# Performance work log

Measured on AMD Instinct MI355X. Metric: run time of the kernel, lower is better.

Reference implementation:

```python
import jax, jax.numpy as jnp
import numpy as np

B, H, S, D = 4, 16, 2048, 128

def setup_inputs() -> dict:
    key = jax.random.key(0)
    kq, kk, kv = jax.random.split(key, 3)
    query = jax.random.normal(kq, (B, H, S, D), dtype=jnp.float32)
    k = jax.random.normal(kk, (B, H, S, D), dtype=jnp.float32)
    value = jax.random.normal(kv, (B, H, S, D), dtype=jnp.float32)
    attn_mask = jnp.zeros((B, H, S, S), dtype=jnp.float32)
    return {"query": query, "key": k, "value": value, "attn_mask": attn_mask}

def reference(query, key, value, attn_mask):
    # scores: [B,H,S,S]
    scale = 1.0 / jnp.sqrt(jnp.asarray(query.shape[-1], query.dtype))
    scores = jnp.einsum('bhqd,bhkd->bhqk', query, key) * scale + attn_mask
    attn = jax.nn.softmax(scores, axis=-1)
    out = jnp.einsum('bhqk,bhkd->bhqd', attn, value)
    return out
```

## Files before the change

### kernel.cpp

```cpp
#include <hip/hip_runtime.h>

#define SDIM 2048
#define DDIM 128
#define NBH  64
#define BR   128
#define BC   64
#define PSTRIDE 72

using bf16x8 = __attribute__((ext_vector_type(8))) short;
using f32x4  = __attribute__((ext_vector_type(4))) float;

static __device__ __forceinline__ short f2bf(float x) {
    unsigned u = __float_as_uint(x);
    u += 0x7fff + ((u >> 16) & 1);
    return (short)(u >> 16);
}
static __device__ __forceinline__ unsigned pack2(float a, float b) {
    return ((unsigned)(unsigned short)f2bf(a)) |
           (((unsigned)(unsigned short)f2bf(b)) << 16);
}

__global__ __launch_bounds__(256) void kconv_kernel(const float* __restrict__ K,
                                                    unsigned short* __restrict__ Kc)
{
    size_t i = ((size_t)blockIdx.x * 256 + threadIdx.x) * 4;
    float4 v = *(const float4*)(K + i);
    uint2 o;
    o.x = pack2(v.x, v.y);
    o.y = pack2(v.z, v.w);
    *(uint2*)(Kc + i) = o;
}

__global__ __launch_bounds__(256) void vtrans_kernel(const float* __restrict__ V,
                                                     unsigned short* __restrict__ Vt)
{
    __shared__ float t[32][33];
    const int bh = blockIdx.z;
    const int s0 = blockIdx.x * 32;
    const int d0 = blockIdx.y * 32;
    const int x = threadIdx.x & 31;
    const int y = threadIdx.x >> 5;
    const float* Vb = V + (size_t)bh * SDIM * DDIM;
    unsigned short* Vtb = Vt + (size_t)bh * SDIM * DDIM;
#pragma unroll
    for (int i = 0; i < 4; ++i) {
        int r = y + i * 8;
        t[r][x] = Vb[(size_t)(s0 + r) * DDIM + d0 + x];
    }
    __syncthreads();
#pragma unroll
    for (int i = 0; i < 4; ++i) {
        int r = y + i * 8;
        Vtb[(size_t)(d0 + r) * SDIM + s0 + x] = (unsigned short)f2bf(t[x][r]);
    }
}

__global__ __launch_bounds__(256, 2) void fattn_kernel(
    const float* __restrict__ Q, const float* __restrict__ M,
    const unsigned short* __restrict__ Kc, const unsigned short* __restrict__ Vt,
    float* __restrict__ O)
{
    const int qt   = blockIdx.x;
    const int bh   = blockIdx.y;
    const int tid  = threadIdx.x;
    const int wave = tid >> 6;
    const int lane = tid & 63;
    const int quad = lane >> 4;
    const int n16  = lane & 15;
    const int q0   = qt * BR;

    const float* Qb = Q + (size_t)bh * SDIM * DDIM;
    const float* Mb = M + (size_t)bh * SDIM * SDIM;
    const unsigned short* Kb = Kc + (size_t)bh * SDIM * DDIM;
    const unsigned short* Vb = Vt + (size_t)bh * SDIM * DDIM;
    float* Ob = O + (size_t)bh * SDIM * DDIM;

    __shared__ __align__(16) unsigned short Ps[4][32 * PSTRIDE];

    const float scale = 0.08838834764831845f;
    bf16x8 qf[2][4];
#pragma unroll
    for (int rt = 0; rt < 2; ++rt) {
        int row = q0 + wave * 32 + rt * 16 + n16;
        const float* qp = Qb + (size_t)row * DDIM + quad * 8;
#pragma unroll
        for (int dt = 0; dt < 4; ++dt) {
            const float* p = qp + dt * 32;
            float4 a = *(const float4*)p;
            float4 b = *(const float4*)(p + 4);
            bf16x8 f;
            f[0] = f2bf(a.x * scale); f[1] = f2bf(a.y * scale);
            f[2] = f2bf(a.z * scale); f[3] = f2bf(a.w * scale);
            f[4] = f2bf(b.x * scale); f[5] = f2bf(b.y * scale);
            f[6] = f2bf(b.z * scale); f[7] = f2bf(b.w * scale);
            qf[rt][dt] = f;
        }
    }

    f32x4 acc[2][8];
    const f32x4 zero4 = {0.f, 0.f, 0.f, 0.f};
#pragma unroll
    for (int rt = 0; rt < 2; ++rt)
#pragma unroll
        for (int nt = 0; nt < 8; ++nt) acc[rt][nt] = zero4;
    float mrow[2][4], lrow[2][4];
#pragma unroll
    for (int rt = 0; rt < 2; ++rt)
#pragma unroll
        for (int r = 0; r < 4; ++r) { mrow[rt][r] = -1e30f; lrow[rt][r] = 0.f; }

    for (int k0 = 0; k0 < SDIM; k0 += BC) {
        float mk[2][4][4];
#pragma unroll
        for (int rt = 0; rt < 2; ++rt) {
            int rowb = q0 + wave * 32 + rt * 16 + quad * 4;
            const float* mpb = Mb + (size_t)rowb * SDIM + k0 + n16;
#pragma unroll
            for (int ct = 0; ct < 4; ++ct)
#pragma unroll
                for (int r = 0; r < 4; ++r)
                    mk[rt][ct][r] = mpb[(size_t)r * SDIM + ct * 16];
        }

        f32x4 s[2][4];
#pragma unroll
        for (int rt = 0; rt < 2; ++rt)
#pragma unroll
            for (int ct = 0; ct < 4; ++ct) s[rt][ct] = zero4;
#pragma unroll
        for (int dt = 0; dt < 4; ++dt) {
#pragma unroll
            for (int ct = 0; ct < 4; ++ct) {
                bf16x8 kf = *(const bf16x8*)(Kb + (size_t)(k0 + ct * 16 + n16) * DDIM + dt * 32 + quad * 8);
                s[0][ct] = __builtin_amdgcn_mfma_f32_16x16x32_bf16(qf[0][dt], kf, s[0][ct], 0, 0, 0);
                s[1][ct] = __builtin_amdgcn_mfma_f32_16x16x32_bf16(qf[1][dt], kf, s[1][ct], 0, 0, 0);
            }
        }

#pragma unroll
        for (int rt = 0; rt < 2; ++rt)
#pragma unroll
            for (int ct = 0; ct < 4; ++ct)
#pragma unroll
                for (int r = 0; r < 4; ++r)
                    s[rt][ct][r] += mk[rt][ct][r];

        float mx[2][4];
#pragma unroll
        for (int rt = 0; rt < 2; ++rt)
#pragma unroll
            for (int r = 0; r < 4; ++r)
                mx[rt][r] = fmaxf(fmaxf(s[rt][0][r], s[rt][1][r]),
                                  fmaxf(s[rt][2][r], s[rt][3][r]));
#pragma unroll
        for (int st = 1; st <= 8; st <<= 1)
#pragma unroll
            for (int rt = 0; rt < 2; ++rt)
#pragma unroll
                for (int r = 0; r < 4; ++r)
                    mx[rt][r] = fmaxf(mx[rt][r], __shfl_xor(mx[rt][r], st));

        float al[2][4], rs[2][4];
#pragma unroll
        for (int rt = 0; rt < 2; ++rt)
#pragma unroll
            for (int r = 0; r < 4; ++r) {
                float mnew = fmaxf(mrow[rt][r], mx[rt][r]);
                al[rt][r] = exp2f((mrow[rt][r] - mnew) * 1.44269504f);
                mrow[rt][r] = mnew;
                float t = 0.f;
#pragma unroll
                for (int ct = 0; ct < 4; ++ct) {
                    float pv = exp2f((s[rt][ct][r] - mnew) * 1.44269504f);
                    s[rt][ct][r] = pv;
                    t += pv;
                }
                rs[rt][r] = t;
            }
#pragma unroll
        for (int st = 1; st <= 8; st <<= 1)
#pragma unroll
            for (int rt = 0; rt < 2; ++rt)
#pragma unroll
                for (int r = 0; r < 4; ++r)
                    rs[rt][r] += __shfl_xor(rs[rt][r], st);
#pragma unroll
        for (int rt = 0; rt < 2; ++rt)
#pragma unroll
            for (int r = 0; r < 4; ++r) {
                lrow[rt][r] = lrow[rt][r] * al[rt][r] + rs[rt][r];
#pragma unroll
                for (int nt = 0; nt < 8; ++nt) acc[rt][nt][r] *= al[rt][r];
            }

#pragma unroll
        for (int rt = 0; rt < 2; ++rt)
#pragma unroll
            for (int ct = 0; ct < 4; ++ct)
#pragma unroll
                for (int r = 0; r < 4; ++r)
                    Ps[wave][(rt * 16 + (lane >> 4) * 4 + r) * PSTRIDE + ct * 16 + n16] =
                        (unsigned short)f2bf(s[rt][ct][r]);

        bf16x8 pa[2][2];
#pragma unroll
        for (int rt = 0; rt < 2; ++rt)
#pragma unroll
            for (int kt = 0; kt < 2; ++kt)
                pa[rt][kt] = *(const bf16x8*)(&Ps[wave][(rt * 16 + n16) * PSTRIDE + kt * 32 + quad * 8]);

#pragma unroll
        for (int nt = 0; nt < 8; ++nt) {
#pragma unroll
            for (int kt = 0; kt < 2; ++kt) {
                bf16x8 vf = *(const bf16x8*)(Vb + (size_t)(nt * 16 + n16) * SDIM + k0 + kt * 32 + quad * 8);
                acc[0][nt] = __builtin_amdgcn_mfma_f32_16x16x32_bf16(pa[0][kt], vf, acc[0][nt], 0, 0, 0);
                acc[1][nt] = __builtin_amdgcn_mfma_f32_16x16x32_bf16(pa[1][kt], vf, acc[1][nt], 0, 0, 0);
            }
        }
    }

#pragma unroll
    for (int rt = 0; rt < 2; ++rt) {
#pragma unroll
        for (int r = 0; r < 4; ++r) {
            float inv = 1.0f / lrow[rt][r];
            int row = q0 + wave * 32 + rt * 16 + quad * 4 + r;
            float* op = Ob + (size_t)row * DDIM + n16;
#pragma unroll
            for (int nt = 0; nt < 8; ++nt)
                op[nt * 16] = acc[rt][nt][r] * inv;
        }
    }
}

extern "C" void kernel_launch(void* const* d_in, const int* in_sizes, int n_in,
                              void* d_out, int out_size, void* d_ws, size_t ws_size,
                              hipStream_t stream) {
    const float* Q = (const float*)d_in[0];
    const float* K = (const float*)d_in[1];
    const float* V = (const float*)d_in[2];
    const float* M = (const float*)d_in[3];
    float* O = (float*)d_out;

    unsigned short* Kc = (unsigned short*)d_ws;
    unsigned short* Vt = Kc + (size_t)NBH * SDIM * DDIM;

    size_t nElem = (size_t)NBH * SDIM * DDIM;
    kconv_kernel<<<dim3(nElem / (256 * 4)), 256, 0, stream>>>(K, Kc);
    vtrans_kernel<<<dim3(SDIM / 32, DDIM / 32, NBH), 256, 0, stream>>>(V, Vt);

    dim3 grid(SDIM / BR, NBH);
    fattn_kernel<<<grid, 256, 0, stream>>>(Q, M, Kc, Vt, O);
}
```

Measured before the change: 1.974 ms.

## Prefetch mask tiles one step ahead, skip unchanged-max rescale, remap grid for locality

Measured after the change: 1.983 ms. About the same (+0.5%).

```diff
diff --git a/kernel.cpp b/kernel.cpp
--- a/kernel.cpp
+++ b/kernel.cpp
@@ -55,13 +55,159 @@
     }
 }
 
+static __device__ __forceinline__ void load_mask(const float* __restrict__ Mb,
+                                                 int q0, int wave, int quad, int n16,
+                                                 int kcol, float (&mk)[2][4][4])
+{
+#pragma unroll
+    for (int rt = 0; rt < 2; ++rt) {
+        const int rowb = q0 + wave * 32 + rt * 16 + quad * 4;
+        const float* mpb = Mb + (size_t)rowb * SDIM + kcol + n16;
+#pragma unroll
+        for (int ct = 0; ct < 4; ++ct)
+#pragma unroll
+            for (int r = 0; r < 4; ++r)
+                mk[rt][ct][r] = mpb[(size_t)r * SDIM + ct * 16];
+    }
+}
+
+static __device__ __forceinline__ void ktile_body(
+    int k0, int q0, int wave, int quad, int n16, int lane,
+    const float* __restrict__ Mb,
+    const unsigned short* __restrict__ Kb, const unsigned short* __restrict__ Vb,
+    unsigned short* __restrict__ PsW,
+    const bf16x8 (&qf)[2][4],
+    f32x4 (&acc)[2][8], float (&mrow)[2][4], float (&lrow)[2][4],
+    float (&mkc)[2][4][4], float (&mkn)[2][4][4])
+{
+    const f32x4 zero4 = {0.f, 0.f, 0.f, 0.f};
+
+    f32x4 s[2][4];
+#pragma unroll
+    for (int rt = 0; rt < 2; ++rt)
+#pragma unroll
+        for (int ct = 0; ct < 4; ++ct) s[rt][ct] = zero4;
+#pragma unroll
+    for (int dt = 0; dt < 4; ++dt) {
+#pragma unroll
+        for (int ct = 0; ct < 4; ++ct) {
+            bf16x8 kf = *(const bf16x8*)(Kb + (size_t)(k0 + ct * 16 + n16) * DDIM + dt * 32 + quad * 8);
+            s[0][ct] = __builtin_amdgcn_mfma_f32_16x16x32_bf16(qf[0][dt], kf, s[0][ct], 0, 0, 0);
+            s[1][ct] = __builtin_amdgcn_mfma_f32_16x16x32_bf16(qf[1][dt], kf, s[1][ct], 0, 0, 0);
+        }
+    }
+
+    __builtin_amdgcn_sched_barrier(0);
+    load_mask(Mb, q0, wave, quad, n16, (k0 + BC) & (SDIM - 1), mkn);
+    __builtin_amdgcn_sched_barrier(0);
+
+#pragma unroll
+    for (int rt = 0; rt < 2; ++rt)
+#pragma unroll
+        for (int ct = 0; ct < 4; ++ct)
+#pragma unroll
+            for (int r = 0; r < 4; ++r)
+                s[rt][ct][r] += mkc[rt][ct][r];
+
+    float mx[2][4];
+#pragma unroll
+    for (int rt = 0; rt < 2; ++rt)
+#pragma unroll
+        for (int r = 0; r < 4; ++r)
+            mx[rt][r] = fmaxf(fmaxf(s[rt][0][r], s[rt][1][r]),
+                              fmaxf(s[rt][2][r], s[rt][3][r]));
+#pragma unroll
+    for (int st = 1; st <= 8; st <<= 1)
+#pragma unroll
+        for (int rt = 0; rt < 2; ++rt)
+#pragma unroll
+            for (int r = 0; r < 4; ++r)
+                mx[rt][r] = fmaxf(mx[rt][r], __shfl_xor(mx[rt][r], st));
+
+    int anynew = 0;
+#pragma unroll
+    for (int rt = 0; rt < 2; ++rt)
+#pragma unroll
+        for (int r = 0; r < 4; ++r)
+            anynew |= (mx[rt][r] > mrow[rt][r]) ? 1 : 0;
+    if (__ballot(anynew) != 0ull) {
+#pragma unroll
+        for (int rt = 0; rt < 2; ++rt)
+#pragma unroll
+            for (int r = 0; r < 4; ++r) {
+                float mnew = fmaxf(mrow[rt][r], mx[rt][r]);
+                float al = exp2f((mrow[rt][r] - mnew) * 1.44269504f);
+                mrow[rt][r] = mnew;
+                lrow[rt][r] *= al;
+#pragma unroll
+                for (int nt = 0; nt < 8; ++nt) acc[rt][nt][r] *= al;
+            }
+    }
+
+    float rs[2][4];
+#pragma unroll
+    for (int rt = 0; rt < 2; ++rt)
+#pragma unroll
+        for (int r = 0; r < 4; ++r) {
+            float t = 0.f;
+#pragma unroll
+            for (int ct = 0; ct < 4; ++ct) {
+                float pv = exp2f((s[rt][ct][r] - mrow[rt][r]) * 1.44269504f);
+                s[rt][ct][r] = pv;
+                t += pv;
+            }
+            rs[rt][r] = t;
+        }
+#pragma unroll
+    for (int st = 1; st <= 8; st <<= 1)
+#pragma unroll
+        for (int rt = 0; rt < 2; ++rt)
+#pragma unroll
+            for (int r = 0; r < 4; ++r)
+                rs[rt][r] += __shfl_xor(rs[rt][r], st);
+#pragma unroll
+    for (int rt = 0; rt < 2; ++rt)
+#pragma unroll
+        for (int r = 0; r < 4; ++r)
+            lrow[rt][r] += rs[rt][r];
+
+#pragma unroll
+    for (int rt = 0; rt < 2; ++rt)
+#pragma unroll
+        for (int ct = 0; ct < 4; ++ct)
+#pragma unroll
+            for (int r = 0; r < 4; ++r)
+                PsW[(rt * 16 + (lane >> 4) * 4 + r) * PSTRIDE + ct * 16 + n16] =
+                    (unsigned short)f2bf(s[rt][ct][r]);
+
+    bf16x8 pa[2][2];
+#pragma unroll
+    for (int rt = 0; rt < 2; ++rt)
+#pragma unroll
+        for (int kt = 0; kt < 2; ++kt)
+            pa[rt][kt] = *(const bf16x8*)(&PsW[(rt * 16 + n16) * PSTRIDE + kt * 32 + quad * 8]);
+
+#pragma unroll
+    for (int nt = 0; nt < 8; ++nt) {
+#pragma unroll
+        for (int kt = 0; kt < 2; ++kt) {
+            bf16x8 vf = *(const bf16x8*)(Vb + (size_t)(nt * 16 + n16) * SDIM + k0 + kt * 32 + quad * 8);
+            acc[0][nt] = __builtin_amdgcn_mfma_f32_16x16x32_bf16(pa[0][kt], vf, acc[0][nt], 0, 0, 0);
+            acc[1][nt] = __builtin_amdgcn_mfma_f32_16x16x32_bf16(pa[1][kt], vf, acc[1][nt], 0, 0, 0);
+        }
+    }
+}
+
 __global__ __launch_bounds__(256, 2) void fattn_kernel(
     const float* __restrict__ Q, const float* __restrict__ M,
     const unsigned short* __restrict__ Kc, const unsigned short* __restrict__ Vt,
     float* __restrict__ O)
 {
-    const int qt   = blockIdx.x;
-    const int bh   = blockIdx.y;
+    const int flat = blockIdx.x;
+    const int slot = flat >> 3;
+    const int bh   = (flat & 7) * 8 + (slot >> 4);
+    const int qt   = slot & 15;
+
     const int tid  = threadIdx.x;
     const int wave = tid >> 6;
     const int lane = tid & 63;
@@ -76,6 +222,7 @@
     float* Ob = O + (size_t)bh * SDIM * DDIM;
 
     __shared__ __align__(16) unsigned short Ps[4][32 * PSTRIDE];
+    unsigned short* PsW = Ps[wave];
 
     const float scale = 0.08838834764831845f;
     bf16x8 qf[2][4];
@@ -109,115 +256,15 @@
 #pragma unroll
         for (int r = 0; r < 4; ++r) { mrow[rt][r] = -1e30f; lrow[rt][r] = 0.f; }
 
-    for (int k0 = 0; k0 < SDIM; k0 += BC) {
-        float mk[2][4][4];
-#pragma unroll
-        for (int rt = 0; rt < 2; ++rt) {
-            int rowb = q0 + wave * 32 + rt * 16 + quad * 4;
-            const float* mpb = Mb + (size_t)rowb * SDIM + k0 + n16;
-#pragma unroll
-            for (int ct = 0; ct < 4; ++ct)
-#pragma unroll
-                for (int r = 0; r < 4; ++r)
-                    mk[rt][ct][r] = mpb[(size_t)r * SDIM + ct * 16];
-        }
-
-        f32x4 s[2][4];
-#pragma unroll
-        for (int rt = 0; rt < 2; ++rt)
-#pragma unroll
-            for (int ct = 0; ct < 4; ++ct) s[rt][ct] = zero4;
-#pragma unroll
-        for (int dt = 0; dt < 4; ++dt) {
-#pragma unroll
-            for (int ct = 0; ct < 4; ++ct) {
-                bf16x8 kf = *(const bf16x8*)(Kb + (size_t)(k0 + ct * 16 + n16) * DDIM + dt * 32 + quad * 8);
-                s[0][ct] = __builtin_amdgcn_mfma_f32_16x16x32_bf16(qf[0][dt], kf, s[0][ct], 0, 0, 0);
-                s[1][ct] = __builtin_amdgcn_mfma_f32_16x16x32_bf16(qf[1][dt], kf, s[1][ct], 0, 0, 0);
-            }
-        }
-
-#pragma unroll
-        for (int rt = 0; rt < 2; ++rt)
-#pragma unroll
-            for (int ct = 0; ct < 4; ++ct)
-#pragma unroll
-                for (int r = 0; r < 4; ++r)
-                    s[rt][ct][r] += mk[rt][ct][r];
-
-        float mx[2][4];
-#pragma unroll
-        for (int rt = 0; rt < 2; ++rt)
-#pragma unroll
-            for (int r = 0; r < 4; ++r)
-                mx[rt][r] = fmaxf(fmaxf(s[rt][0][r], s[rt][1][r]),
-                                  fmaxf(s[rt][2][r], s[rt][3][r]));
-#pragma unroll
-        for (int st = 1; st <= 8; st <<= 1)
-#pragma unroll
-            for (int rt = 0; rt < 2; ++rt)
-#pragma unroll
-                for (int r = 0; r < 4; ++r)
-                    mx[rt][r] = fmaxf(mx[rt][r], __shfl_xor(mx[rt][r], st));
-
-        float al[2][4], rs[2][4];
-#pragma unroll
-        for (int rt = 0; rt < 2; ++rt)
-#pragma unroll
-            for (int r = 0; r < 4; ++r) {
-                float mnew = fmaxf(mrow[rt][r], mx[rt][r]);
-                al[rt][r] = exp2f((mrow[rt][r] - mnew) * 1.44269504f);
-                mrow[rt][r] = mnew;
-                float t = 0.f;
-#pragma unroll
-                for (int ct = 0; ct < 4; ++ct) {
-                    float pv = exp2f((s[rt][ct][r] - mnew) * 1.44269504f);
-                    s[rt][ct][r] = pv;
-                    t += pv;
-                }
-                rs[rt][r] = t;
-            }
-#pragma unroll
-        for (int st = 1; st <= 8; st <<= 1)
-#pragma unroll
-            for (int rt = 0; rt < 2; ++rt)
-#pragma unroll
-                for (int r = 0; r < 4; ++r)
-                    rs[rt][r] += __shfl_xor(rs[rt][r], st);
-#pragma unroll
-        for (int rt = 0; rt < 2; ++rt)
-#pragma unroll
-            for (int r = 0; r < 4; ++r) {
-                lrow[rt][r] = lrow[rt][r] * al[rt][r] + rs[rt][r];
-#pragma unroll
-                for (int nt = 0; nt < 8; ++nt) acc[rt][nt][r] *= al[rt][r];
-            }
-
-#pragma unroll
-        for (int rt = 0; rt < 2; ++rt)
-#pragma unroll
-            for (int ct = 0; ct < 4; ++ct)
-#pragma unroll
-                for (int r = 0; r < 4; ++r)
-                    Ps[wave][(rt * 16 + (lane >> 4) * 4 + r) * PSTRIDE + ct * 16 + n16] =
-                        (unsigned short)f2bf(s[rt][ct][r]);
-
-        bf16x8 pa[2][2];
-#pragma unroll
-        for (int rt = 0; rt < 2; ++rt)
-#pragma unroll
-            for (int kt = 0; kt < 2; ++kt)
-                pa[rt][kt] = *(const bf16x8*)(&Ps[wave][(rt * 16 + n16) * PSTRIDE + kt * 32 + quad * 8]);
-
-#pragma unroll
-        for (int nt = 0; nt < 8; ++nt) {
-#pragma unroll
-            for (int kt = 0; kt < 2; ++kt) {
-                bf16x8 vf = *(const bf16x8*)(Vb + (size_t)(nt * 16 + n16) * SDIM + k0 + kt * 32 + quad * 8);
-                acc[0][nt] = __builtin_amdgcn_mfma_f32_16x16x32_bf16(pa[0][kt], vf, acc[0][nt], 0, 0, 0);
-                acc[1][nt] = __builtin_amdgcn_mfma_f32_16x16x32_bf16(pa[1][kt], vf, acc[1][nt], 0, 0, 0);
-            }
-        }
+    float mkA[2][4][4], mkB[2][4][4];
+    load_mask(Mb, q0, wave, quad, n16, 0, mkA);
+
+#pragma unroll 1
+    for (int k0 = 0; k0 < SDIM; k0 += 2 * BC) {
+        ktile_body(k0,      q0, wave, quad, n16, lane, Mb, Kb, Vb, PsW,
+                   qf, acc, mrow, lrow, mkA, mkB);
+        ktile_body(k0 + BC, q0, wave, quad, n16, lane, Mb, Kb, Vb, PsW,
+                   qf, acc, mrow, lrow, mkB, mkA);
     }
 
 #pragma unroll
@@ -250,6 +297,5 @@
     kconv_kernel<<<dim3(nElem / (256 * 4)), 256, 0, stream>>>(K, Kc);
     vtrans_kernel<<<dim3(SDIM / 32, DDIM / 32, NBH), 256, 0, stream>>>(V, Vt);
 
-    dim3 grid(SDIM / BR, NBH);
-    fattn_kernel<<<grid, 256, 0, stream>>>(Q, M, Kc, Vt, O);
-}
+    fattn_kernel<<<dim3((SDIM / BR) * NBH), 256, 0, stream>>>(Q, M, Kc, Vt, O);
+}
```
